# Kernel optimization log

Hardware: AMD Instinct MI355X
Metric: run time of the kernel (lower is better)

Reference implementation:

```python
import jax, jax.numpy as jnp
import numpy as np
import math

B, M, N = 2, 512, 2048
CI = 256          # input_pts_channel == hidden for fuse_method='ADD'
HID = 256
HEADS = 8
DH = HID // HEADS
INTER = 1024
L = 4
EPS = 1e-5


def _ln(x, g, b):
    m = jnp.mean(x, -1, keepdims=True)
    v = jnp.mean((x - m) ** 2, -1, keepdims=True)
    return (x - m) / jnp.sqrt(v + EPS) * g + b


def _sinenc(dims, coords):
    # coords: (B, P) -> (B, P, dims); even channels sin, odd channels cos
    h = jnp.arange(dims)
    inv = jnp.power(10000.0, (h // 2) * 2.0 / dims)
    c = coords[..., None] / inv
    return jnp.where(h % 2 == 0, jnp.sin(c), jnp.cos(c))


def setup_inputs() -> dict:
    key = jax.random.key(0)
    ks = jax.random.split(key, 32)
    it = iter(ks)
    def nrm(shape, s=1.0):
        return jax.random.normal(next(it), shape, dtype=jnp.float32) * s
    inp = {
        'query_c2d': nrm((B, M, 2), 10.0),
        'query_f2d': nrm((B, M, CI)),
        'query_f3d': nrm((B, M, CI)),
        'key_c2d': nrm((B, N, 2), 10.0),
        'key_f2d': nrm((B, N, CI)),
        'key_f3d': nrm((B, N, CI)),
        'attn_mask': jax.random.bernoulli(next(it), 0.9, (B, N)),
        'ln1_g': jnp.ones((CI,)), 'ln1_b': jnp.zeros((CI,)),
        'dc_W': nrm((CI, HID), 0.02), 'dc_b': jnp.zeros((HID,)),
        'dcln_g': jnp.ones((HID,)), 'dcln_b': jnp.zeros((HID,)),
        'cls_f3d': nrm((HID,)),
        'Wq': nrm((L, HID, HID), 0.02), 'bq': jnp.zeros((L, HID)),
        'Wk': nrm((L, HID, HID), 0.02), 'bk': jnp.zeros((L, HID)),
        'Wv': nrm((L, HID, HID), 0.02), 'bv': jnp.zeros((L, HID)),
        'Wd': nrm((L, HID, HID), 0.02), 'bd': jnp.zeros((L, HID)),
        'aln_g': jnp.ones((L, HID)), 'aln_b': jnp.zeros((L, HID)),
        'W1': nrm((L, HID, INTER), 0.02), 'b1': jnp.zeros((L, INTER)),
        'W2': nrm((L, INTER, HID), 0.02), 'b2': jnp.zeros((L, HID)),
        'fln_g': jnp.ones((L, HID)), 'fln_b': jnp.zeros((L, HID)),
    }
    return inp


def _forward(qc2, qf2, qf3, kc2, kf2, kf3, mask,
             ln1_g, ln1_b, dc_W, dc_b, dcln_g, dcln_b, cls_f3d,
             Wq, bq, Wk, bk, Wv, bv, Wd, bd, aln_g, aln_b,
             W1, b1, W2, b2, fln_g, fln_b):
    def sh(x):  # (B,P,HID) -> (B,H,P,DH)
        return x.reshape(x.shape[0], x.shape[1], HEADS, DH).transpose(0, 2, 1, 3)

    def layer(i, q_in, k_in, m, query_self):
        Qh = sh(q_in @ Wq[i] + bq[i])
        Kh = sh(k_in @ Wk[i] + bk[i])
        Vh = sh(k_in @ Wv[i] + bv[i])
        scores = jnp.einsum('bhmd,bhnd->bhmn', Qh, Kh)
        if m is not None:
            scores = scores - (~m).astype(scores.dtype)[:, None, None, :] * 1e10
        if query_self:
            SKh = sh(q_in @ Wk[i] + bk[i])
            SVh = sh(q_in @ Wv[i] + bv[i])
            sself = jnp.sum(Qh * SKh, -1, keepdims=True)  # (B,H,M,1)
            scores = jnp.concatenate([sself, scores], -1)
        probs = jax.nn.softmax(scores / math.sqrt(DH), -1)
        if query_self:
            sp, probs = probs[..., :1], probs[..., 1:]
        o = jnp.einsum('bhmn,bhnd->bhmd', probs, Vh)
        if query_self:
            o = o + sp * SVh
        o = o.transpose(0, 2, 1, 3).reshape(q_in.shape[0], q_in.shape[1], HID)
        a = _ln(o @ Wd[i] + bd[i] + q_in, aln_g[i], aln_b[i])
        f = jax.nn.relu(a @ W1[i] + b1[i]) @ W2[i] + b2[i]
        return _ln(f + a, fln_g[i], fln_b[i])

    qc = jnp.concatenate([_sinenc(CI // 2, qc2[:, :, 0]), _sinenc(CI // 2, qc2[:, :, 1])], -1)
    kc = jnp.concatenate([_sinenc(CI // 2, kc2[:, :, 0]), _sinenc(CI // 2, kc2[:, :, 1])], -1)
    qs = _ln(_ln(qf2 + qf3 + qc, ln1_g, ln1_b) @ dc_W + dc_b, dcln_g, dcln_b)
    ks = _ln(_ln(kf2 + kf3 + kc, ln1_g, ln1_b) @ dc_W + dc_b, dcln_g, dcln_b)
    cls = jnp.broadcast_to(cls_f3d[None, None, :], (qs.shape[0], 1, HID))
    for i in range(L):
        ks = layer(i, ks, ks, mask, False)
        qs = layer(i, qs, ks, mask, True)
        cls = layer(i, cls, jnp.concatenate([cls, ks, qs], 1), None, False)
    return qs, ks, cls


def reference(query_c2d, query_f2d, query_f3d, key_c2d, key_f2d, key_f3d, attn_mask,
              ln1_g, ln1_b, dc_W, dc_b, dcln_g, dcln_b, cls_f3d,
              Wq, bq, Wk, bk, Wv, bv, Wd, bd, aln_g, aln_b,
              W1, b1, W2, b2, fln_g, fln_b):
    return _forward(query_c2d, query_f2d, query_f3d, key_c2d, key_f2d, key_f3d, attn_mask,
                    ln1_g, ln1_b, dc_W, dc_b, dcln_g, dcln_b, cls_f3d,
                    Wq, bq, Wk, bk, Wv, bv, Wd, bd, aln_g, aln_b,
                    W1, b1, W2, b2, fln_g, fln_b)
```

## Files before the change

### kernel.cpp

```cpp
#include <hip/hip_runtime.h>
#include <math.h>

namespace {
constexpr int kB = 2;
constexpr int kM = 512;
constexpr int kN = 2048;
constexpr int kHID = 256;
constexpr int kDH = 32;
constexpr int kL = 4;
constexpr float kEPS = 1e-5f;
constexpr int kKV = 2560;
}

typedef __attribute__((ext_vector_type(8))) short short8;
typedef __attribute__((ext_vector_type(4))) float f32x4;

__device__ inline ushort f2b(float f) {
  unsigned u = __builtin_bit_cast(unsigned, f);
  unsigned r = (u + 0x7fffu + ((u >> 16) & 1u)) >> 16;
  return (ushort)r;
}
__device__ inline float b2f(ushort u) {
  return __builtin_bit_cast(float, (unsigned)u << 16);
}
__device__ inline unsigned cvtpk(float lo, float hi) {
  unsigned r;
  asm("v_cvt_pk_bf16_f32 %0, %1, %2" : "=v"(r) : "v"(lo), "v"(hi));
  return r;
}
__device__ inline void gld16(ushort* lds, const ushort* g) {
  __builtin_amdgcn_global_load_lds(
      (const __attribute__((address_space(1))) void*)g,
      (__attribute__((address_space(3))) void*)lds, 16, 0, 0);
}

__device__ inline float dot8(const float* a, short8 w) {
  float s = 0.f;
  #pragma unroll
  for (int jj = 0; jj < 8; ++jj) s += a[jj] * b2f((ushort)w[jj]);
  return s;
}

__global__ __launch_bounds__(256) void mask_norm_kernel(
    const unsigned char* __restrict__ mraw, float* __restrict__ mf)
{
  int tid = threadIdx.x;
  __shared__ unsigned sh[4];
  if (tid < 4) sh[tid] = 0;
  __syncthreads();
  unsigned l1 = 0, l2 = 0, l3 = 0, l4 = 0;
  for (int j = 0; j < 16; ++j) {
    int p = tid * 16 + j;
    unsigned v = mraw[p];
    int r = p & 3;
    if (r == 1) l1 |= v;
    else if (r == 2) l2 |= v;
    else if (r == 3) l3 |= v;
    else if ((p & 7) == 4) l4 |= v;
  }
  if (l1) atomicOr(&sh[0], l1);
  if (l2) atomicOr(&sh[1], l2);
  if (l3) atomicOr(&sh[2], l3);
  if (l4) atomicOr(&sh[3], l4);
  __syncthreads();
  unsigned a1 = sh[0], a2 = sh[1], a3 = sh[2], a4 = sh[3];
  int mode;
  if ((a1 | a2 | a3) == 0) mode = a4 ? 1 : 2;
  else if (a1 == 0 && (a2 & ~0x80u) == 0 && (a3 & ~0x3Fu) == 0 && ((a2 | a3) != 0))
    mode = 3;
  else mode = 0;

  int i = blockIdx.x * 256 + tid;
  unsigned char v;
  if (mode == 0) v = mraw[i];
  else if (mode == 1) v = mraw[i * 4];
  else if (mode == 2) v = mraw[i * 8];
  else v = mraw[i * 4 + 3];
  mf[i] = v ? 0.f : -2.5505654e9f;
}

__global__ __launch_bounds__(256) void encode2_kernel(
    const float* __restrict__ qc2, const float* __restrict__ qf2,
    const float* __restrict__ qf3, const float* __restrict__ kc2,
    const float* __restrict__ kf2, const float* __restrict__ kf3,
    const float* __restrict__ g, const float* __restrict__ bb,
    ushort* __restrict__ out)
{
  int row = blockIdx.x;
  const float *c2d, *f2, *f3;
  int r;
  if (row < kB * kM) { c2d = qc2; f2 = qf2; f3 = qf3; r = row; }
  else { c2d = kc2; f2 = kf2; f3 = kf3; r = row - kB * kM; }
  int c = threadIdx.x;
  float coord = c2d[(size_t)r * 2 + (c >> 7)];
  int h = c & 127;
  float ex = (float)(h & ~1) * (1.0f / 128.0f);
  float inv = expf(ex * 9.210340371976184f);
  float val = coord / inv;
  float e = (h & 1) ? cosf(val) : sinf(val);
  float x = f2[(size_t)r * 256 + c] + f3[(size_t)r * 256 + c] + e;
  __shared__ float red[256];
  red[c] = x; __syncthreads();
  for (int s = 128; s > 0; s >>= 1) { if (c < s) red[c] += red[c + s]; __syncthreads(); }
  float mean = red[0] * (1.0f / 256.0f);
  __syncthreads();
  float d = x - mean;
  red[c] = d * d; __syncthreads();
  for (int s = 128; s > 0; s >>= 1) { if (c < s) red[c] += red[c + s]; __syncthreads(); }
  float var = red[0] * (1.0f / 256.0f);
  out[(size_t)row * 256 + c] = f2b(d * rsqrtf(var + kEPS) * g[c] + bb[c]);
}

struct WJobs {
  const float* W[7]; ushort* Wt[7];
  int K[7], C[7], off[7];
};
__global__ __launch_bounds__(256) void wconv_all_kernel(WJobs J)
{
  __shared__ float t[32][33];
  int bid = blockIdx.x;
  int j = 0;
  #pragma unroll
  for (int q = 1; q < 7; ++q) if (bid >= J.off[q]) j = q;
  int tl = bid - J.off[j];
  int K = J.K[j], C = J.C[j];
  int tpl = (K >> 5) * (C >> 5);
  int layer = tl / tpl, rem = tl - layer * tpl;
  int kt = rem % (K >> 5), ct = rem / (K >> 5);
  const float* Wl = J.W[j] + (size_t)layer * K * C;
  ushort* Wtl = J.Wt[j] + (size_t)layer * K * C;
  int k0 = kt * 32, c0 = ct * 32;
  int tx = threadIdx.x & 31, ty = threadIdx.x >> 5;
  for (int i = ty; i < 32; i += 8) t[i][tx] = Wl[(size_t)(k0 + i) * C + c0 + tx];
  __syncthreads();
  for (int i = ty; i < 32; i += 8)
    Wtl[(size_t)(c0 + i) * K + k0 + tx] = f2b(t[tx][i]);
}

struct GDesc {
  const ushort* A; const ushort* Bt; const float* bias; const float* res; void* out;
  int R, K, C, flags;
  int in_rpb, out_rpb, out_off, vt_stride;
};
struct GBatch { GDesc d[5]; };

__global__ __launch_bounds__(256) void gemmx_kernel(GBatch bt)
{
  GDesc d = bt.d[blockIdx.z];
  int r0 = blockIdx.x * 64;
  if (r0 >= d.R) return;
  int c0 = blockIdx.y * 64;

  __shared__ ushort As[4096];
  __shared__ ushort Bs[4096];
  int tid = threadIdx.x;
  int lam = tid & 63, wv = tid >> 6;
  int wr = wv >> 1, wc = wv & 1;
  int K = d.K;
  int srow8 = lam >> 3;
  int sxor = (lam & 7) ^ srow8;

  f32x4 acc[2][2] = {};

  for (int k0 = 0; k0 < K; k0 += 64) {
    #pragma unroll
    for (int i = 0; i < 2; ++i) {
      int row = 16 * wv + 8 * i + srow8;
      gld16(As + wv * 1024 + i * 512,
            d.A + (size_t)(r0 + row) * K + k0 + 8 * sxor);
      gld16(Bs + wv * 1024 + i * 512,
            d.Bt + (size_t)(c0 + row) * K + k0 + 8 * sxor);
    }
    __syncthreads();
    #pragma unroll
    for (int ks = 0; ks < 2; ++ks) {
      short8 af[2], bf_[2];
      #pragma unroll
      for (int m = 0; m < 2; ++m) {
        int ra = wr * 32 + m * 16 + (lam & 15);
        int ch = (ks * 4 + (lam >> 4)) ^ (ra & 7);
        af[m] = *(const short8*)(As + ra * 64 + ch * 8);
      }
      #pragma unroll
      for (int n = 0; n < 2; ++n) {
        int rb = wc * 32 + n * 16 + (lam & 15);
        int ch = (ks * 4 + (lam >> 4)) ^ (rb & 7);
        bf_[n] = *(const short8*)(Bs + rb * 64 + ch * 8);
      }
      #pragma unroll
      for (int m = 0; m < 2; ++m)
        #pragma unroll
        for (int n = 0; n < 2; ++n)
          acc[m][n] = __builtin_amdgcn_mfma_f32_16x16x32_bf16(
              af[m], bf_[n], acc[m][n], 0, 0, 0);
    }
    __syncthreads();
  }

  if (!(d.flags & 4)) {
    #pragma unroll
    for (int m = 0; m < 2; ++m) {
      #pragma unroll
      for (int reg = 0; reg < 4; ++reg) {
        int gr = r0 + wr * 32 + m * 16 + (lam >> 4) * 4 + reg;
        int bidx = gr / d.in_rpb, rr = gr - bidx * d.in_rpb;
        size_t orow = (size_t)bidx * d.out_rpb + d.out_off + rr;
        #pragma unroll
        for (int n = 0; n < 2; ++n) {
          int gc = c0 + wc * 32 + n * 16 + (lam & 15);
          float v = acc[m][n][reg] + d.bias[gc];
          if (d.res) v += d.res[(size_t)gr * d.C + gc];
          if (d.flags & 1) v = fmaxf(v, 0.f);
          if (d.flags & 2) ((ushort*)d.out)[orow * d.C + gc] = f2b(v);
          else ((float*)d.out)[orow * d.C + gc] = v;
        }
      }
    }
  } else {
    #pragma unroll
    for (int m = 0; m < 2; ++m)
      #pragma unroll
      for (int n = 0; n < 2; ++n)
        #pragma unroll
        for (int reg = 0; reg < 4; ++reg) {
          int col = wc * 32 + n * 16 + (lam & 15);
          int row = wr * 32 + m * 16 + (lam >> 4) * 4 + reg;
          float v = acc[m][n][reg] + d.bias[c0 + col];
          As[col * 64 + (((row >> 3) ^ (col & 7)) << 3) + (row & 7)] = f2b(v);
        }
    __syncthreads();
    int col2 = tid >> 2, rc = tid & 3;
    #pragma unroll
    for (int u = 0; u < 2; ++u) {
      int rowc = rc * 2 + u;
      short8 val = *(const short8*)(As + col2 * 64 + ((rowc ^ (col2 & 7)) << 3));
      int r = r0 + rowc * 8;
      int bidx = r / d.in_rpb, rr = r - bidx * d.in_rpb;
      *(short8*)((ushort*)d.out +
                 ((size_t)bidx * 256 + c0 + col2) * d.vt_stride + d.out_off + rr) = val;
    }
  }
}

__global__ __launch_bounds__(256) void gemmln_kernel(
    const ushort* __restrict__ A, const ushort* __restrict__ Bt,
    const float* __restrict__ bias, const float* __restrict__ res,
    const float* __restrict__ g, const float* __restrict__ bb,
    float* __restrict__ outf, ushort* __restrict__ outb, int R, int K)
{
  __shared__ ushort As[16 * 64];
  __shared__ ushort Bs[256 * 64];
  __shared__ float redL[16][4];
  int r0 = blockIdx.x * 16;
  int tid = threadIdx.x;
  int lam = tid & 63, wv = tid >> 6;
  int srow8 = lam >> 3;
  int sxor = (lam & 7) ^ srow8;

  f32x4 acc[4] = {};

  for (int k0 = 0; k0 < K; k0 += 64) {
    if (wv < 2)
      gld16(As + wv * 512, A + (size_t)(r0 + wv * 8 + srow8) * K + k0 + 8 * sxor);
    #pragma unroll
    for (int j = 0; j < 8; ++j) {
      int cc = wv * 8 + j;
      gld16(Bs + cc * 512, Bt + (size_t)(cc * 8 + srow8) * K + k0 + 8 * sxor);
    }
    __syncthreads();
    #pragma unroll
    for (int ks = 0; ks < 2; ++ks) {
      int ra = lam & 15;
      int cha = (ks * 4 + (lam >> 4)) ^ (ra & 7);
      short8 af = *(const short8*)(As + ra * 64 + cha * 8);
      #pragma unroll
      for (int cg = 0; cg < 4; ++cg) {
        int rb = wv * 64 + cg * 16 + (lam & 15);
        int chb = (ks * 4 + (lam >> 4)) ^ (rb & 7);
        short8 bf_ = *(const short8*)(Bs + rb * 64 + chb * 8);
        acc[cg] = __builtin_amdgcn_mfma_f32_16x16x32_bf16(af, bf_, acc[cg], 0, 0, 0);
      }
    }
    __syncthreads();
  }

  int col_lo = lam & 15, rsel = lam >> 4;
  float v[4][4];
  #pragma unroll
  for (int cg = 0; cg < 4; ++cg) {
    int col = wv * 64 + cg * 16 + col_lo;
    float bi = bias[col];
    #pragma unroll
    for (int reg = 0; reg < 4; ++reg) {
      int row = r0 + rsel * 4 + reg;
      float x = acc[cg][reg] + bi;
      if (res) x += res[(size_t)row * 256 + col];
      v[cg][reg] = x;
    }
  }
  float mean[4];
  {
    float ps[4];
    #pragma unroll
    for (int reg = 0; reg < 4; ++reg) {
      ps[reg] = v[0][reg] + v[1][reg] + v[2][reg] + v[3][reg];
      #pragma unroll
      for (int o = 1; o < 16; o <<= 1) ps[reg] += __shfl_xor(ps[reg], o);
    }
    if (col_lo == 0)
      #pragma unroll
      for (int reg = 0; reg < 4; ++reg) redL[rsel * 4 + reg][wv] = ps[reg];
    __syncthreads();
    #pragma unroll
    for (int reg = 0; reg < 4; ++reg) {
      int rr = rsel * 4 + reg;
      mean[reg] = (redL[rr][0] + redL[rr][1] + redL[rr][2] + redL[rr][3]) * (1.0f / 256.0f);
    }
    __syncthreads();
  }
  float rs_[4];
  {
    float ps[4];
    #pragma unroll
    for (int reg = 0; reg < 4; ++reg) {
      float s = 0.f;
      #pragma unroll
      for (int cg = 0; cg < 4; ++cg) {
        float dd = v[cg][reg] - mean[reg];
        s += dd * dd;
      }
      ps[reg] = s;
      #pragma unroll
      for (int o = 1; o < 16; o <<= 1) ps[reg] += __shfl_xor(ps[reg], o);
    }
    if (col_lo == 0)
      #pragma unroll
      for (int reg = 0; reg < 4; ++reg) redL[rsel * 4 + reg][wv] = ps[reg];
    __syncthreads();
    #pragma unroll
    for (int reg = 0; reg < 4; ++reg) {
      int rr = rsel * 4 + reg;
      float var = (redL[rr][0] + redL[rr][1] + redL[rr][2] + redL[rr][3]) * (1.0f / 256.0f);
      rs_[reg] = rsqrtf(var + kEPS);
    }
  }
  #pragma unroll
  for (int cg = 0; cg < 4; ++cg) {
    int col = wv * 64 + cg * 16 + col_lo;
    float gg = g[col], bv = bb[col];
    #pragma unroll
    for (int reg = 0; reg < 4; ++reg) {
      int row = r0 + rsel * 4 + reg;
      float y = (v[cg][reg] - mean[reg]) * rs_[reg] * gg + bv;
      outf[(size_t)row * 256 + col] = y;
      outb[(size_t)row * 256 + col] = f2b(y);
    }
  }
}

__global__ __launch_bounds__(256) void attn6_kernel(
    const ushort* __restrict__ Qp, const ushort* __restrict__ Kp,
    const ushort* __restrict__ Vt, float* __restrict__ Pp,
    const float* __restrict__ madd,
    int Sq, int k_rpb, int vt_stride, int self_off, int slen, int ns)
{
  __shared__ ushort KsL[64 * 32];
  __shared__ ushort VtL[32 * 64];
  int bh = blockIdx.x;
  int b = bh >> 3, h = bh & 7;
  int sidx = blockIdx.z;
  int tid = threadIdx.x;
  int lane = tid & 63;
  int qlane = lane & 15, g = lane >> 4;
  int gq = blockIdx.y * 64 + (tid >> 6) * 16 + qlane;
  const float scale2 = 0.17677669529663688f * 1.4426950408889634f;

  short8 qB = *(const short8*)(Qp + ((size_t)(b * Sq + gq)) * 256 + h * 32 + g * 8);

  float mi = -3.0e38f, li = 0.f;
  f32x4 acc0 = {}, acc1 = {};

  if (self_off >= 0 && sidx == 0) {
    const ushort* kr = Kp + ((size_t)(b * k_rpb + self_off + gq)) * 256 + h * 32 + g * 8;
    short8 k8 = *(const short8*)kr;
    float part = 0.f;
    #pragma unroll
    for (int j = 0; j < 8; ++j) part += b2f((ushort)qB[j]) * b2f((ushort)k8[j]);
    part += __shfl_xor(part, 16);
    part += __shfl_xor(part, 32);
    mi = part * scale2;
    li = 1.f;
    const ushort* vb = Vt + ((size_t)(b * 256 + h * 32)) * vt_stride + self_off + gq;
    #pragma unroll
    for (int r = 0; r < 4; ++r) {
      acc0[r] = b2f(vb[(size_t)(4 * g + r) * vt_stride]);
      acc1[r] = b2f(vb[(size_t)(16 + 4 * g + r) * vt_stride]);
    }
  }

  const float* mb = madd + (size_t)b * kN;
  int skey = tid >> 2, sc = tid & 3;
  int sd = tid >> 3, sc8 = tid & 7;
  const ushort* Ksrc = Kp + ((size_t)(b * k_rpb + skey)) * 256 + h * 32 + sc * 8;
  const ushort* Vsrc = Vt + ((size_t)(b * 256 + h * 32 + sd)) * vt_stride + sc8 * 8;
  ushort* Kdst = KsL + skey * 32 + ((sc ^ ((skey >> 1) & 3)) << 3);
  ushort* Vdst = VtL + sd * 64 + ((sc8 ^ (sd & 7)) << 3);

  int base = sidx * slen;
  int ntile = slen >> 6;

  for (int it = 0; it < ntile; ++it) {
    int n0 = base + it * 64;
    __syncthreads();
    *(short8*)Kdst = *(const short8*)(Ksrc + (size_t)n0 * 256);
    *(short8*)Vdst = *(const short8*)(Vsrc + n0);
    __syncthreads();

    float4 m4[4];
    #pragma unroll
    for (int f = 0; f < 4; ++f)
      m4[f] = *(const float4*)(mb + n0 + 16 * f + 4 * g);

    f32x4 st[4];
    __builtin_amdgcn_s_setprio(1);
    #pragma unroll
    for (int f = 0; f < 4; ++f) {
      int key = f * 16 + qlane;
      short8 kf = *(const short8*)(KsL + key * 32 + ((g ^ ((key >> 1) & 3)) << 3));
      st[f] = __builtin_amdgcn_mfma_f32_16x16x32_bf16(
          kf, qB, (f32x4){0.f, 0.f, 0.f, 0.f}, 0, 0, 0);
    }
    __builtin_amdgcn_s_setprio(0);

    float p[4][4];
    float tm = -3.0e38f;
    #pragma unroll
    for (int f = 0; f < 4; ++f) {
      float mm[4] = {m4[f].x, m4[f].y, m4[f].z, m4[f].w};
      #pragma unroll
      for (int r = 0; r < 4; ++r) {
        float s = fmaf(st[f][r], scale2, mm[r]);
        p[f][r] = s;
        tm = fmaxf(tm, s);
      }
    }
    tm = fmaxf(tm, __shfl_xor(tm, 16));
    tm = fmaxf(tm, __shfl_xor(tm, 32));
    if (__any(tm > mi + 11.5f)) {
      float nm = fmaxf(mi, tm);
      float fs = exp2f(mi - nm);
      li *= fs; mi = nm;
      #pragma unroll
      for (int r = 0; r < 4; ++r) { acc0[r] *= fs; acc1[r] *= fs; }
    }
    float ls = 0.f;
    #pragma unroll
    for (int f = 0; f < 4; ++f)
      #pragma unroll
      for (int r = 0; r < 4; ++r) {
        float pv = exp2f(p[f][r] - mi);
        p[f][r] = pv;
        ls += pv;
      }
    ls += __shfl_xor(ls, 16);
    ls += __shfl_xor(ls, 32);
    li += ls;

    unsigned pkw[4][2];
    #pragma unroll
    for (int f = 0; f < 4; ++f) {
      pkw[f][0] = cvtpk(p[f][0], p[f][1]);
      pkw[f][1] = cvtpk(p[f][2], p[f][3]);
    }
    int src0 = qlane | ((2 * (g & 1)) << 4);
    int src1 = src0 + 16;
    bool hi = g >= 2;
    #pragma unroll
    for (int t = 0; t < 2; ++t) {
      unsigned t0 = (unsigned)__shfl((int)pkw[2 * t][0], src0);
      unsigned t1 = (unsigned)__shfl((int)pkw[2 * t][1], src0);
      unsigned t2 = (unsigned)__shfl((int)pkw[2 * t][0], src1);
      unsigned t3 = (unsigned)__shfl((int)pkw[2 * t][1], src1);
      unsigned u0 = (unsigned)__shfl((int)pkw[2 * t + 1][0], src0);
      unsigned u1 = (unsigned)__shfl((int)pkw[2 * t + 1][1], src0);
      unsigned u2 = (unsigned)__shfl((int)pkw[2 * t + 1][0], src1);
      unsigned u3 = (unsigned)__shfl((int)pkw[2 * t + 1][1], src1);
      union { unsigned u[4]; short8 v; } pb;
      pb.u[0] = hi ? u0 : t0;
      pb.u[1] = hi ? u1 : t1;
      pb.u[2] = hi ? u2 : t2;
      pb.u[3] = hi ? u3 : t3;
      __builtin_amdgcn_s_setprio(1);
      int d0 = qlane, d1 = 16 + qlane;
      short8 vf0 = *(const short8*)(VtL + d0 * 64 + (((t * 4 + g) ^ (d0 & 7)) << 3));
      acc0 = __builtin_amdgcn_mfma_f32_16x16x32_bf16(vf0, pb.v, acc0, 0, 0, 0);
      short8 vf1 = *(const short8*)(VtL + d1 * 64 + (((t * 4 + g) ^ (d1 & 7)) << 3));
      acc1 = __builtin_amdgcn_mfma_f32_16x16x32_bf16(vf1, pb.v, acc1, 0, 0, 0);
      __builtin_amdgcn_s_setprio(0);
    }
  }

  float* rec = Pp + ((size_t)(bh * Sq + gq) * ns + sidx) * 20;
  if (g == 0) { rec[0] = mi; rec[1] = li; }
  ushort* accp = (ushort*)(rec + 2);
  uint2 w0, w1;
  w0.x = cvtpk(acc0[0], acc0[1]); w0.y = cvtpk(acc0[2], acc0[3]);
  w1.x = cvtpk(acc1[0], acc1[1]); w1.y = cvtpk(acc1[2], acc1[3]);
  *(uint2*)(accp + 4 * g) = w0;
  *(uint2*)(accp + 16 + 4 * g) = w1;
}

__global__ __launch_bounds__(256) void combine_kernel(
    const float* __restrict__ Pp, ushort* __restrict__ AO, int Sq, int ns)
{
  int r = blockIdx.x * 8 + (threadIdx.x >> 5);
  int d = threadIdx.x & 31;
  int bh = r / Sq, q = r - bh * Sq;
  int b = bh >> 3, h = bh & 7;
  const float* rb = Pp + (size_t)r * ns * 20;
  float M = -3.0e38f;
  for (int s2 = 0; s2 < ns; ++s2) M = fmaxf(M, rb[s2 * 20]);
  float L = 0.f, O = 0.f;
  for (int s2 = 0; s2 < ns; ++s2) {
    float w = exp2f(rb[s2 * 20] - M);
    L += rb[s2 * 20 + 1] * w;
    O += w * b2f(((const ushort*)(rb + s2 * 20 + 2))[d]);
  }
  AO[((size_t)(b * Sq + q)) * 256 + h * 32 + d] = f2b(O / L);
}

__global__ __launch_bounds__(256) void cls_attn_kernel(
    const float* __restrict__ cls_s,
    const ushort* __restrict__ WqT, const float* __restrict__ bq,
    const ushort* __restrict__ WkT, const float* __restrict__ bk,
    const ushort* __restrict__ WvT, const float* __restrict__ bv,
    const ushort* __restrict__ Kbig, const ushort* __restrict__ Vt,
    float* __restrict__ AOc)
{
  __shared__ float c0f[256], qv[32], k0v[32], v0v[32];
  __shared__ float red[256];
  __shared__ float sarr[2560];
  __shared__ float scl[4];
  const float scale2 = 0.17677669529663688f * 1.4426950408889634f;
  int b = blockIdx.x >> 3, h = blockIdx.x & 7;
  int t = threadIdx.x;
  c0f[t] = cls_s[b * 256 + t];
  __syncthreads();

  const ushort* Wm[3] = {WqT, WkT, WvT};
  const float* Bi[3] = {bq, bk, bv};
  float* Ov[3] = {qv, k0v, v0v};
  for (int pi = 0; pi < 3; ++pi) {
    int d = t >> 3, sl = t & 7;
    const ushort* wrow = Wm[pi] + (size_t)(h * 32 + d) * 256 + sl * 32;
    float part = 0.f;
    #pragma unroll
    for (int j = 0; j < 32; j += 8) {
      short8 w8 = *(const short8*)(wrow + j);
      #pragma unroll
      for (int jj = 0; jj < 8; ++jj) part += c0f[sl * 32 + j + jj] * b2f((ushort)w8[jj]);
    }
    red[t] = part;
    __syncthreads();
    if (t < 32) {
      float sum = 0.f;
      #pragma unroll
      for (int s = 0; s < 8; ++s) sum += red[t * 8 + s];
      Ov[pi][t] = sum + Bi[pi][h * 32 + t];
    }
    __syncthreads();
  }

  if (t < 32) red[t] = qv[t] * k0v[t];
  __syncthreads();
  if (t == 0) {
    float sc = 0.f;
    for (int j = 0; j < 32; ++j) sc += red[j];
    scl[0] = sc * scale2;
  }
  __syncthreads();

  float lmax = -3.0e38f;
  for (int it = 0; it < 10; ++it) {
    int key = t + it * 256;
    const ushort* krow = Kbig + ((size_t)(b * kKV + key)) * 256 + h * 32;
    float sdot = 0.f;
    #pragma unroll
    for (int j = 0; j < 4; ++j) {
      short8 k8 = ((const short8*)krow)[j];
      #pragma unroll
      for (int jj = 0; jj < 8; ++jj) sdot += qv[j * 8 + jj] * b2f((ushort)k8[jj]);
    }
    sdot *= scale2;
    sarr[key] = sdot;
    lmax = fmaxf(lmax, sdot);
  }
  red[t] = lmax;
  __syncthreads();
  for (int s = 128; s > 0; s >>= 1) { if (t < s) red[t] = fmaxf(red[t], red[t + s]); __syncthreads(); }
  if (t == 0) scl[1] = fmaxf(red[0], scl[0]);
  __syncthreads();
  float M = scl[1];
  float lsum = 0.f;
  for (int it = 0; it < 10; ++it) {
    int key = t + it * 256;
    float pv = exp2f(sarr[key] - M);
    sarr[key] = pv;
    lsum += pv;
  }
  red[t] = lsum;
  __syncthreads();
  for (int s = 128; s > 0; s >>= 1) { if (t < s) red[t] += red[t + s]; __syncthreads(); }
  if (t == 0) {
    scl[3] = exp2f(scl[0] - M);
    scl[2] = red[0] + scl[3];
  }
  __syncthreads();

  {
    int d = t & 31, sl = t >> 5;
    const ushort* vrow = Vt + ((size_t)(b * 256 + h * 32 + d)) * kKV + sl * 320;
    float acc = 0.f;
    for (int j = 0; j < 320; j += 8) {
      short8 v8 = *(const short8*)(vrow + j);
      #pragma unroll
      for (int jj = 0; jj < 8; ++jj) acc += sarr[sl * 320 + j + jj] * b2f((ushort)v8[jj]);
    }
    red[sl * 32 + d] = acc;
  }
  __syncthreads();
  if (t < 32) {
    float o = scl[3] * v0v[t];
    #pragma unroll
    for (int s = 0; s < 8; ++s) o += red[s * 32 + t];
    AOc[b * 256 + h * 32 + t] = o / scl[2];
  }
}

__device__ inline float blk_sum1024(float v, float* red, int t) {
  red[t] = v; __syncthreads();
  for (int s = 512; s > 0; s >>= 1) {
    if (t < s) red[t] += red[t + s];
    __syncthreads();
  }
  float r = red[0];
  __syncthreads();
  return r;
}

__global__ __launch_bounds__(1024) void cls_mlp_kernel(
    const float* __restrict__ AOc, float* __restrict__ cls_s,
    const ushort* __restrict__ WdT, const float* __restrict__ bd,
    const float* __restrict__ ag, const float* __restrict__ ab,
    const ushort* __restrict__ W1T, const float* __restrict__ b1,
    const ushort* __restrict__ W2T, const float* __restrict__ b2,
    const float* __restrict__ fg, const float* __restrict__ fb)
{
  __shared__ float oL[256], r0L[256], aL[256], ffL[1024], vL[256], red[1024];
  int b = blockIdx.x, t = threadIdx.x;
  if (t < 256) { oL[t] = AOc[b * 256 + t]; r0L[t] = cls_s[b * 256 + t]; }
  __syncthreads();

  int r8 = t >> 3, c8 = t & 7;
  #pragma unroll
  for (int p = 0; p < 2; ++p) {
    int row = p * 128 + r8;
    const ushort* wr_ = WdT + (size_t)row * 256 + c8 * 8;
    float a0 = 0.f, a1 = 0.f, a2 = 0.f, a3 = 0.f;
    a0 = dot8(oL + c8 * 8, *(const short8*)(wr_));
    a1 = dot8(oL + c8 * 8 + 64, *(const short8*)(wr_ + 64));
    a2 = dot8(oL + c8 * 8 + 128, *(const short8*)(wr_ + 128));
    a3 = dot8(oL + c8 * 8 + 192, *(const short8*)(wr_ + 192));
    float s = (a0 + a1) + (a2 + a3);
    s += __shfl_xor(s, 1);
    s += __shfl_xor(s, 2);
    s += __shfl_xor(s, 4);
    if (c8 == 0) vL[row] = s + bd[row] + r0L[row];
  }
  __syncthreads();
  {
    float x = (t < 256) ? vL[t] : 0.f;
    float mean = blk_sum1024(x, red, t) * (1.0f / 256.0f);
    float d = (t < 256) ? (vL[t] - mean) : 0.f;
    float var = blk_sum1024(d * d, red, t) * (1.0f / 256.0f);
    float rs = rsqrtf(var + kEPS);
    if (t < 256) aL[t] = d * rs * ag[t] + ab[t];
  }
  __syncthreads();
  #pragma unroll
  for (int p = 0; p < 8; ++p) {
    int row = p * 128 + r8;
    const ushort* w1r = W1T + (size_t)row * 256 + c8 * 8;
    float a0 = dot8(aL + c8 * 8, *(const short8*)(w1r));
    float a1 = dot8(aL + c8 * 8 + 64, *(const short8*)(w1r + 64));
    float a2 = dot8(aL + c8 * 8 + 128, *(const short8*)(w1r + 128));
    float a3 = dot8(aL + c8 * 8 + 192, *(const short8*)(w1r + 192));
    float s = (a0 + a1) + (a2 + a3);
    s += __shfl_xor(s, 1);
    s += __shfl_xor(s, 2);
    s += __shfl_xor(s, 4);
    if (c8 == 0) ffL[row] = fmaxf(s + b1[row], 0.f);
  }
  __syncthreads();
  #pragma unroll
  for (int p = 0; p < 2; ++p) {
    int row = p * 128 + r8;
    const ushort* w2r = W2T + (size_t)row * 1024 + c8 * 8;
    float a0 = 0.f, a1 = 0.f, a2 = 0.f, a3 = 0.f;
    #pragma unroll
    for (int j = 0; j < 1024; j += 256) {
      a0 += dot8(ffL + c8 * 8 + j, *(const short8*)(w2r + j));
      a1 += dot8(ffL + c8 * 8 + j + 64, *(const short8*)(w2r + j + 64));
      a2 += dot8(ffL + c8 * 8 + j + 128, *(const short8*)(w2r + j + 128));
      a3 += dot8(ffL + c8 * 8 + j + 192, *(const short8*)(w2r + j + 192));
    }
    float s = (a0 + a1) + (a2 + a3);
    s += __shfl_xor(s, 1);
    s += __shfl_xor(s, 2);
    s += __shfl_xor(s, 4);
    if (c8 == 0) vL[row] = s + b2[row] + aL[row];
  }
  __syncthreads();
  {
    float x = (t < 256) ? vL[t] : 0.f;
    float mean = blk_sum1024(x, red, t) * (1.0f / 256.0f);
    float d = (t < 256) ? (vL[t] - mean) : 0.f;
    float var = blk_sum1024(d * d, red, t) * (1.0f / 256.0f);
    float rs = rsqrtf(var + kEPS);
    if (t < 256) cls_s[b * 256 + t] = d * rs * fg[t] + fb[t];
  }
}

__global__ void cls_init_kernel(const float* __restrict__ cf, float* __restrict__ cls)
{
  int i = blockIdx.x * 256 + threadIdx.x;
  cls[i] = cf[i & 255];
}

__global__ __launch_bounds__(256) void copyout_kernel(
    const float* __restrict__ qs, const float* __restrict__ ks,
    const float* __restrict__ cls, float* __restrict__ out)
{
  int i = blockIdx.x * 256 + threadIdx.x;
  float v;
  if (i < 262144) v = qs[i];
  else if (i < 1310720) v = ks[i - 262144];
  else v = cls[i - 1310720];
  out[i] = v;
}

extern "C" void kernel_launch(void* const* d_in, const int* in_sizes, int n_in,
                              void* d_out, int out_size, void* d_ws, size_t ws_size,
                              hipStream_t stream)
{
  const float* qc2    = (const float*)d_in[0];
  const float* qf2    = (const float*)d_in[1];
  const float* qf3    = (const float*)d_in[2];
  const float* kc2    = (const float*)d_in[3];
  const float* kf2    = (const float*)d_in[4];
  const float* kf3    = (const float*)d_in[5];
  const unsigned char* mraw = (const unsigned char*)d_in[6];
  const float* ln1_g  = (const float*)d_in[7];
  const float* ln1_b  = (const float*)d_in[8];
  const float* dc_W   = (const float*)d_in[9];
  const float* dc_b   = (const float*)d_in[10];
  const float* dcln_g = (const float*)d_in[11];
  const float* dcln_b = (const float*)d_in[12];
  const float* cls_f  = (const float*)d_in[13];
  const float* Wq     = (const float*)d_in[14];
  const float* bq     = (const float*)d_in[15];
  const float* Wk     = (const float*)d_in[16];
  const float* bk     = (const float*)d_in[17];
  const float* Wv     = (const float*)d_in[18];
  const float* bv     = (const float*)d_in[19];
  const float* Wd     = (const float*)d_in[20];
  const float* bd     = (const float*)d_in[21];
  const float* aln_g  = (const float*)d_in[22];
  const float* aln_b  = (const float*)d_in[23];
  const float* W1     = (const float*)d_in[24];
  const float* b1     = (const float*)d_in[25];
  const float* W2     = (const float*)d_in[26];
  const float* b2     = (const float*)d_in[27];
  const float* fln_g  = (const float*)d_in[28];
  const float* fln_b  = (const float*)d_in[29];

  float* ws = (float*)d_ws;
  float* maskf = ws + 0;
  float* qs_s  = ws + 4096;
  float* ks_s  = ws + 266240;
  float* cls_s = ws + 1314816;
  float* AOc   = ws + 1315328;
  float* Scr   = ws + 1316864;
  float* Ta    = Scr;
  float* ksPart = Scr + 1048576;
  float* qsPart = Scr + 1048576;
  ushort* ub   = (ushort*)(ws + 4986880);
  ushort* qs_b   = ub + 0;
  ushort* ks_b   = ub + 262144;
  ushort* T2b    = ub + 1310720;
  ushort* Kbig   = ub + 2359296;
  ushort* Vt_ks  = ub + 3670016;
  ushort* Vt_big = ub + 4718592;
  ushort* FFb    = ub + 6029312;
  ushort* encT   = FFb + 0;
  ushort* Qb     = FFb + 0;
  ushort* Kks    = FFb + 1048576;
  ushort* AOb    = FFb + 2097152;
  ushort* wts    = ub + 10223616;
  ushort* dcWt = wts;
  ushort* WqT  = wts + 65536;
  ushort* WkT  = WqT + 262144;
  ushort* WvT  = WkT + 262144;
  ushort* WdT  = WvT + 262144;
  ushort* W1T  = WdT + 262144;
  ushort* W2T  = W1T + 1048576;

  auto mk = [](const ushort* A, const ushort* Bt, const float* bias, const float* res,
               void* out, int R, int K, int C, int flags,
               int in_rpb, int out_rpb, int out_off, int vt_stride) {
    GDesc g; g.A = A; g.Bt = Bt; g.bias = bias; g.res = res; g.out = out;
    g.R = R; g.K = K; g.C = C; g.flags = flags; g.in_rpb = in_rpb;
    g.out_rpb = out_rpb; g.out_off = out_off; g.vt_stride = vt_stride; return g;
  };
  auto launch = [&](const GDesc* ds, int n) {
    GBatch bt{};
    int maxR = 0;
    for (int i = 0; i < n; ++i) { bt.d[i] = ds[i]; if (ds[i].R > maxR) maxR = ds[i].R; }
    gemmx_kernel<<<dim3(maxR / 64, ds[0].C / 64, n), 256, 0, stream>>>(bt);
  };
  auto gln = [&](const ushort* A, const ushort* Bt, const float* bias, const float* res,
                 const float* g_, const float* b_, float* of, ushort* ob, int R, int K) {
    gemmln_kernel<<<R / 16, 256, 0, stream>>>(A, Bt, bias, res, g_, b_, of, ob, R, K);
  };

  mask_norm_kernel<<<16, 256, 0, stream>>>(mraw, maskf);

  {
    WJobs J;
    const float* Ws[7] = {dc_W, Wq, Wk, Wv, Wd, W1, W2};
    ushort* Ts[7] = {dcWt, WqT, WkT, WvT, WdT, W1T, W2T};
    int Ks[7] = {256, 256, 256, 256, 256, 256, 1024};
    int Cs[7] = {256, 256, 256, 256, 256, 1024, 256};
    int Ls[7] = {1, 4, 4, 4, 4, 4, 4};
    int off = 0;
    for (int j = 0; j < 7; ++j) {
      J.W[j] = Ws[j]; J.Wt[j] = Ts[j]; J.K[j] = Ks[j]; J.C[j] = Cs[j]; J.off[j] = off;
      off += (Ks[j] / 32) * (Cs[j] / 32) * Ls[j];
    }
    wconv_all_kernel<<<off, 256, 0, stream>>>(J);
  }

  encode2_kernel<<<kB * (kM + kN), 256, 0, stream>>>(qc2, qf2, qf3, kc2, kf2, kf3,
                                                     ln1_g, ln1_b, encT);
  gln(encT, dcWt, dc_b, nullptr, dcln_g, dcln_b, qs_s, qs_b, kB * (kM + kN), 256);
  cls_init_kernel<<<2, 256, 0, stream>>>(cls_f, cls_s);

  for (int i = 0; i < kL; ++i) {
    const ushort* Wq_i = WqT + (size_t)i * 65536;  const float* bq_i = bq + i * 256;
    const ushort* Wk_i = WkT + (size_t)i * 65536;  const float* bk_i = bk + i * 256;
    const ushort* Wv_i = WvT + (size_t)i * 65536;  const float* bv_i = bv + i * 256;
    const ushort* Wd_i = WdT + (size_t)i * 65536;  const float* bd_i = bd + i * 256;
    const float* ag_i = aln_g + i * 256;           const float* ab_i = aln_b + i * 256;
    const ushort* W1_i = W1T + (size_t)i * 262144; const float* b1_i = b1 + i * 1024;
    const ushort* W2_i = W2T + (size_t)i * 262144; const float* b2_i = b2 + i * 256;
    const float* fg_i = fln_g + i * 256;           const float* fb_i = fln_b + i * 256;
    int Rk = kB * kN, Rq = kB * kM;

    {
      GDesc ds[3] = {
        mk(ks_b, Wq_i, bq_i, nullptr, Qb,  Rk, 256, 256, 2, Rk, Rk, 0, 0),
        mk(ks_b, Wk_i, bk_i, nullptr, Kks, Rk, 256, 256, 2, Rk, Rk, 0, 0),
        mk(ks_b, Wv_i, bv_i, nullptr, Vt_ks, Rk, 256, 256, 4, kN, 0, 0, kN)};
      launch(ds, 3);
    }
    attn6_kernel<<<dim3(kB * 8, kN / 64, 4), 256, 0, stream>>>(
        Qb, Kks, Vt_ks, ksPart, maskf, kN, kN, kN, -1, kN / 4, 4);
    combine_kernel<<<kB * 8 * kN / 8, 256, 0, stream>>>(ksPart, AOb, kN, 4);
    gln(AOb, Wd_i, bd_i, ks_s, ag_i, ab_i, Ta, T2b, Rk, 256);
    { GDesc d = mk(T2b, W1_i, b1_i, nullptr, FFb, Rk, 256, 1024, 1 | 2, Rk, Rk, 0, 0);
      launch(&d, 1); }
    gln(FFb, W2_i, b2_i, Ta, fg_i, fb_i, ks_s, ks_b, Rk, 1024);

    {
      GDesc ds[5] = {
        mk(qs_b, Wq_i, bq_i, nullptr, Qb, Rq, 256, 256, 2, Rq, Rq, 0, 0),
        mk(ks_b, Wk_i, bk_i, nullptr, Kbig, Rk, 256, 256, 2, kN, kKV, 0, 0),
        mk(ks_b, Wv_i, bv_i, nullptr, Vt_big, Rk, 256, 256, 4, kN, 0, 0, kKV),
        mk(qs_b, Wk_i, bk_i, nullptr, Kbig, Rq, 256, 256, 2, kM, kKV, kN, 0),
        mk(qs_b, Wv_i, bv_i, nullptr, Vt_big, Rq, 256, 256, 4, kM, 0, kN, kKV)};
      launch(ds, 5);
    }
    attn6_kernel<<<dim3(kB * 8, kM / 64, 4), 256, 0, stream>>>(
        Qb, Kbig, Vt_big, qsPart, maskf, kM, kKV, kKV, kN, kN / 4, 4);
    combine_kernel<<<kB * 8 * kM / 8, 256, 0, stream>>>(qsPart, AOb, kM, 4);
    gln(AOb, Wd_i, bd_i, qs_s, ag_i, ab_i, Ta, T2b, Rq, 256);
    { GDesc d = mk(T2b, W1_i, b1_i, nullptr, FFb, Rq, 256, 1024, 1 | 2, Rq, Rq, 0, 0);
      launch(&d, 1); }
    gln(FFb, W2_i, b2_i, Ta, fg_i, fb_i, qs_s, qs_b, Rq, 1024);

    {
      GDesc ds[2] = {
        mk(qs_b, Wk_i, bk_i, nullptr, Kbig, Rq, 256, 256, 2, kM, kKV, kN, 0),
        mk(qs_b, Wv_i, bv_i, nullptr, Vt_big, Rq, 256, 256, 4, kM, 0, kN, kKV)};
      launch(ds, 2);
    }
    cls_attn_kernel<<<16, 256, 0, stream>>>(cls_s, Wq_i, bq_i, Wk_i,
                                            bk_i, Wv_i, bv_i,
                                            Kbig, Vt_big, AOc);
    cls_mlp_kernel<<<2, 1024, 0, stream>>>(AOc, cls_s, Wd_i, bd_i, ag_i, ab_i,
                                           W1_i, b1_i, W2_i, b2_i, fg_i, fb_i);
  }

  copyout_kernel<<<5122, 256, 0, stream>>>(qs_s, ks_s, cls_s, (float*)d_out);
}
```

Baseline: 831.6 us.

## Process two query groups per wave to reuse K/V tiles in attention

The attention kernel now gives each wave two 16-query groups, so a block covers 128 queries and each K/V tile staged in LDS feeds twice as many MFMAs. This halves the number of blocks and the global-to-LDS traffic per query. The query-side attention also raises its KV split count from 4 to 8 to keep the grid large, with the combine step adjusted to match. The cost is roughly double the accumulator and score registers, which may lower occupancy, plus more partial records to merge for the query attention.

After: 837.7 us. No clear change (+0.7%).

```diff
diff --git a/kernel.cpp b/kernel.cpp
--- a/kernel.cpp
+++ b/kernel.cpp
@@ -358,7 +358,7 @@
   }
 }
 
-__global__ __launch_bounds__(256) void attn6_kernel(
+__global__ __launch_bounds__(256) void attn8_kernel(
     const ushort* __restrict__ Qp, const ushort* __restrict__ Kp,
     const ushort* __restrict__ Vt, float* __restrict__ Pp,
     const float* __restrict__ madd,
@@ -372,29 +372,48 @@
   int tid = threadIdx.x;
   int lane = tid & 63;
   int qlane = lane & 15, g = lane >> 4;
-  int gq = blockIdx.y * 64 + (tid >> 6) * 16 + qlane;
+  int gqA = blockIdx.y * 128 + (tid >> 6) * 16 + qlane;
+  int gqB = gqA + 64;
   const float scale2 = 0.17677669529663688f * 1.4426950408889634f;
 
-  short8 qB = *(const short8*)(Qp + ((size_t)(b * Sq + gq)) * 256 + h * 32 + g * 8);
-
-  float mi = -3.0e38f, li = 0.f;
-  f32x4 acc0 = {}, acc1 = {};
+  short8 qBa = *(const short8*)(Qp + ((size_t)(b * Sq + gqA)) * 256 + h * 32 + g * 8);
+  short8 qBb = *(const short8*)(Qp + ((size_t)(b * Sq + gqB)) * 256 + h * 32 + g * 8);
+
+  float miA = -3.0e38f, liA = 0.f, miB = -3.0e38f, liB = 0.f;
+  f32x4 a0A = {}, a1A = {}, a0B = {}, a1B = {};
 
   if (self_off >= 0 && sidx == 0) {
-    const ushort* kr = Kp + ((size_t)(b * k_rpb + self_off + gq)) * 256 + h * 32 + g * 8;
-    short8 k8 = *(const short8*)kr;
-    float part = 0.f;
-    #pragma unroll
-    for (int j = 0; j < 8; ++j) part += b2f((ushort)qB[j]) * b2f((ushort)k8[j]);
-    part += __shfl_xor(part, 16);
-    part += __shfl_xor(part, 32);
-    mi = part * scale2;
-    li = 1.f;
-    const ushort* vb = Vt + ((size_t)(b * 256 + h * 32)) * vt_stride + self_off + gq;
-    #pragma unroll
-    for (int r = 0; r < 4; ++r) {
-      acc0[r] = b2f(vb[(size_t)(4 * g + r) * vt_stride]);
-      acc1[r] = b2f(vb[(size_t)(16 + 4 * g + r) * vt_stride]);
+    {
+      const ushort* kr = Kp + ((size_t)(b * k_rpb + self_off + gqA)) * 256 + h * 32 + g * 8;
+      short8 k8 = *(const short8*)kr;
+      float part = 0.f;
+      #pragma unroll
+      for (int j = 0; j < 8; ++j) part += b2f((ushort)qBa[j]) * b2f((ushort)k8[j]);
+      part += __shfl_xor(part, 16);
+      part += __shfl_xor(part, 32);
+      miA = part * scale2; liA = 1.f;
+      const ushort* vb = Vt + ((size_t)(b * 256 + h * 32)) * vt_stride + self_off + gqA;
+      #pragma unroll
+      for (int r = 0; r < 4; ++r) {
+        a0A[r] = b2f(vb[(size_t)(4 * g + r) * vt_stride]);
+        a1A[r] = b2f(vb[(size_t)(16 + 4 * g + r) * vt_stride]);
+      }
+    }
+    {
+      const ushort* kr = Kp + ((size_t)(b * k_rpb + self_off + gqB)) * 256 + h * 32 + g * 8;
+      short8 k8 = *(const short8*)kr;
+      float part = 0.f;
+      #pragma unroll
+      for (int j = 0; j < 8; ++j) part += b2f((ushort)qBb[j]) * b2f((ushort)k8[j]);
+      part += __shfl_xor(part, 16);
+      part += __shfl_xor(part, 32);
+      miB = part * scale2; liB = 1.f;
+      const ushort* vb = Vt + ((size_t)(b * 256 + h * 32)) * vt_stride + self_off + gqB;
+      #pragma unroll
+      for (int r = 0; r < 4; ++r) {
+        a0B[r] = b2f(vb[(size_t)(4 * g + r) * vt_stride]);
+        a1B[r] = b2f(vb[(size_t)(16 + 4 * g + r) * vt_stride]);
+      }
     }
   }
 
@@ -409,6 +428,10 @@
   int base = sidx * slen;
   int ntile = slen >> 6;
 
+  int src0 = qlane | ((2 * (g & 1)) << 4);
+  int src1 = src0 + 16;
+  bool hi = g >= 2;
+
   for (int it = 0; it < ntile; ++it) {
     int n0 = base + it * 64;
     __syncthreads();
@@ -421,93 +444,164 @@
     for (int f = 0; f < 4; ++f)
       m4[f] = *(const float4*)(mb + n0 + 16 * f + 4 * g);
 
-    f32x4 st[4];
+    f32x4 stA[4], stB[4];
     __builtin_amdgcn_s_setprio(1);
     #pragma unroll
     for (int f = 0; f < 4; ++f) {
       int key = f * 16 + qlane;
       short8 kf = *(const short8*)(KsL + key * 32 + ((g ^ ((key >> 1) & 3)) << 3));
-      st[f] = __builtin_amdgcn_mfma_f32_16x16x32_bf16(
-          kf, qB, (f32x4){0.f, 0.f, 0.f, 0.f}, 0, 0, 0);
+      stA[f] = __builtin_amdgcn_mfma_f32_16x16x32_bf16(
+          kf, qBa, (f32x4){0.f, 0.f, 0.f, 0.f}, 0, 0, 0);
+      stB[f] = __builtin_amdgcn_mfma_f32_16x16x32_bf16(
+          kf, qBb, (f32x4){0.f, 0.f, 0.f, 0.f}, 0, 0, 0);
     }
     __builtin_amdgcn_s_setprio(0);
 
-    float p[4][4];
-    float tm = -3.0e38f;
-    #pragma unroll
-    for (int f = 0; f < 4; ++f) {
-      float mm[4] = {m4[f].x, m4[f].y, m4[f].z, m4[f].w};
-      #pragma unroll
-      for (int r = 0; r < 4; ++r) {
-        float s = fmaf(st[f][r], scale2, mm[r]);
-        p[f][r] = s;
-        tm = fmaxf(tm, s);
-      }
-    }
-    tm = fmaxf(tm, __shfl_xor(tm, 16));
-    tm = fmaxf(tm, __shfl_xor(tm, 32));
-    if (__any(tm > mi + 11.5f)) {
-      float nm = fmaxf(mi, tm);
-      float fs = exp2f(mi - nm);
-      li *= fs; mi = nm;
-      #pragma unroll
-      for (int r = 0; r < 4; ++r) { acc0[r] *= fs; acc1[r] *= fs; }
-    }
-    float ls = 0.f;
-    #pragma unroll
-    for (int f = 0; f < 4; ++f)
-      #pragma unroll
-      for (int r = 0; r < 4; ++r) {
-        float pv = exp2f(p[f][r] - mi);
-        p[f][r] = pv;
-        ls += pv;
-      }
-    ls += __shfl_xor(ls, 16);
-    ls += __shfl_xor(ls, 32);
-    li += ls;
-
-    unsigned pkw[4][2];
-    #pragma unroll
-    for (int f = 0; f < 4; ++f) {
-      pkw[f][0] = cvtpk(p[f][0], p[f][1]);
-      pkw[f][1] = cvtpk(p[f][2], p[f][3]);
-    }
-    int src0 = qlane | ((2 * (g & 1)) << 4);
-    int src1 = src0 + 16;
-    bool hi = g >= 2;
+    unsigned pkwA[4][2], pkwB[4][2];
+    {
+      float p[4][4];
+      float tm = -3.0e38f;
+      #pragma unroll
+      for (int f = 0; f < 4; ++f) {
+        float mm[4] = {m4[f].x, m4[f].y, m4[f].z, m4[f].w};
+        #pragma unroll
+        for (int r = 0; r < 4; ++r) {
+          float sv = fmaf(stA[f][r], scale2, mm[r]);
+          p[f][r] = sv;
+          tm = fmaxf(tm, sv);
+        }
+      }
+      tm = fmaxf(tm, __shfl_xor(tm, 16));
+      tm = fmaxf(tm, __shfl_xor(tm, 32));
+      if (__any(tm > miA + 11.5f)) {
+        float nm = fmaxf(miA, tm);
+        float fs = exp2f(miA - nm);
+        liA *= fs; miA = nm;
+        #pragma unroll
+        for (int r = 0; r < 4; ++r) { a0A[r] *= fs; a1A[r] *= fs; }
+      }
+      float ls = 0.f;
+      #pragma unroll
+      for (int f = 0; f < 4; ++f)
+        #pragma unroll
+        for (int r = 0; r < 4; ++r) {
+          float pv = exp2f(p[f][r] - miA);
+          p[f][r] = pv;
+          ls += pv;
+        }
+      ls += __shfl_xor(ls, 16);
+      ls += __shfl_xor(ls, 32);
+      liA += ls;
+      #pragma unroll
+      for (int f = 0; f < 4; ++f) {
+        pkwA[f][0] = cvtpk(p[f][0], p[f][1]);
+        pkwA[f][1] = cvtpk(p[f][2], p[f][3]);
+      }
+    }
+    {
+      float p[4][4];
+      float tm = -3.0e38f;
+      #pragma unroll
+      for (int f = 0; f < 4; ++f) {
+        float mm[4] = {m4[f].x, m4[f].y, m4[f].z, m4[f].w};
+        #pragma unroll
+        for (int r = 0; r < 4; ++r) {
+          float sv = fmaf(stB[f][r], scale2, mm[r]);
+          p[f][r] = sv;
+          tm = fmaxf(tm, sv);
+        }
+      }
+      tm = fmaxf(tm, __shfl_xor(tm, 16));
+      tm = fmaxf(tm, __shfl_xor(tm, 32));
+      if (__any(tm > miB + 11.5f)) {
+        float nm = fmaxf(miB, tm);
+        float fs = exp2f(miB - nm);
+        liB *= fs; miB = nm;
+        #pragma unroll
+        for (int r = 0; r < 4; ++r) { a0B[r] *= fs; a1B[r] *= fs; }
+      }
+      float ls = 0.f;
+      #pragma unroll
+      for (int f = 0; f < 4; ++f)
+        #pragma unroll
+        for (int r = 0; r < 4; ++r) {
+          float pv = exp2f(p[f][r] - miB);
+          p[f][r] = pv;
+          ls += pv;
+        }
+      ls += __shfl_xor(ls, 16);
+      ls += __shfl_xor(ls, 32);
+      liB += ls;
+      #pragma unroll
+      for (int f = 0; f < 4; ++f) {
+        pkwB[f][0] = cvtpk(p[f][0], p[f][1]);
+        pkwB[f][1] = cvtpk(p[f][2], p[f][3]);
+      }
+    }
+
     #pragma unroll
     for (int t = 0; t < 2; ++t) {
-      unsigned t0 = (unsigned)__shfl((int)pkw[2 * t][0], src0);
-      unsigned t1 = (unsigned)__shfl((int)pkw[2 * t][1], src0);
-      unsigned t2 = (unsigned)__shfl((int)pkw[2 * t][0], src1);
-      unsigned t3 = (unsigned)__shfl((int)pkw[2 * t][1], src1);
-      unsigned u0 = (unsigned)__shfl((int)pkw[2 * t + 1][0], src0);
-      unsigned u1 = (unsigned)__shfl((int)pkw[2 * t + 1][1], src0);
-      unsigned u2 = (unsigned)__shfl((int)pkw[2 * t + 1][0], src1);
-      unsigned u3 = (unsigned)__shfl((int)pkw[2 * t + 1][1], src1);
-      union { unsigned u[4]; short8 v; } pb;
-      pb.u[0] = hi ? u0 : t0;
-      pb.u[1] = hi ? u1 : t1;
-      pb.u[2] = hi ? u2 : t2;
-      pb.u[3] = hi ? u3 : t3;
+      union { unsigned u[4]; short8 v; } pbA, pbB;
+      {
+        unsigned t0 = (unsigned)__shfl((int)pkwA[2 * t][0], src0);
+        unsigned t1 = (unsigned)__shfl((int)pkwA[2 * t][1], src0);
+        unsigned t2 = (unsigned)__shfl((int)pkwA[2 * t][0], src1);
+        unsigned t3 = (unsigned)__shfl((int)pkwA[2 * t][1], src1);
+        unsigned u0 = (unsigned)__shfl((int)pkwA[2 * t + 1][0], src0);
+        unsigned u1 = (unsigned)__shfl((int)pkwA[2 * t + 1][1], src0);
+        unsigned u2 = (unsigned)__shfl((int)pkwA[2 * t + 1][0], src1);
+        unsigned u3 = (unsigned)__shfl((int)pkwA[2 * t + 1][1], src1);
+        pbA.u[0] = hi ? u0 : t0;
+        pbA.u[1] = hi ? u1 : t1;
+        pbA.u[2] = hi ? u2 : t2;
+        pbA.u[3] = hi ? u3 : t3;
+      }
+      {
+        unsigned t0 = (unsigned)__shfl((int)pkwB[2 * t][0], src0);
+        unsigned t1 = (unsigned)__shfl((int)pkwB[2 * t][1], src0);
+        unsigned t2 = (unsigned)__shfl((int)pkwB[2 * t][0], src1);
+        unsigned t3 = (unsigned)__shfl((int)pkwB[2 * t][1], src1);
+        unsigned u0 = (unsigned)__shfl((int)pkwB[2 * t + 1][0], src0);
+        unsigned u1 = (unsigned)__shfl((int)pkwB[2 * t + 1][1], src0);
+        unsigned u2 = (unsigned)__shfl((int)pkwB[2 * t + 1][0], src1);
+        unsigned u3 = (unsigned)__shfl((int)pkwB[2 * t + 1][1], src1);
+        pbB.u[0] = hi ? u0 : t0;
+        pbB.u[1] = hi ? u1 : t1;
+        pbB.u[2] = hi ? u2 : t2;
+        pbB.u[3] = hi ? u3 : t3;
+      }
       __builtin_amdgcn_s_setprio(1);
       int d0 = qlane, d1 = 16 + qlane;
       short8 vf0 = *(const short8*)(VtL + d0 * 64 + (((t * 4 + g) ^ (d0 & 7)) << 3));
-      acc0 = __builtin_amdgcn_mfma_f32_16x16x32_bf16(vf0, pb.v, acc0, 0, 0, 0);
       short8 vf1 = *(const short8*)(VtL + d1 * 64 + (((t * 4 + g) ^ (d1 & 7)) << 3));
-      acc1 = __builtin_amdgcn_mfma_f32_16x16x32_bf16(vf1, pb.v, acc1, 0, 0, 0);
+      a0A = __builtin_amdgcn_mfma_f32_16x16x32_bf16(vf0, pbA.v, a0A, 0, 0, 0);
+      a1A = __builtin_amdgcn_mfma_f32_16x16x32_bf16(vf1, pbA.v, a1A, 0, 0, 0);
+      a0B = __builtin_amdgcn_mfma_f32_16x16x32_bf16(vf0, pbB.v, a0B, 0, 0, 0);
+      a1B = __builtin_amdgcn_mfma_f32_16x16x32_bf16(vf1, pbB.v, a1B, 0, 0, 0);
       __builtin_amdgcn_s_setprio(0);
     }
   }
 
-  float* rec = Pp + ((size_t)(bh * Sq + gq) * ns + sidx) * 20;
-  if (g == 0) { rec[0] = mi; rec[1] = li; }
-  ushort* accp = (ushort*)(rec + 2);
-  uint2 w0, w1;
-  w0.x = cvtpk(acc0[0], acc0[1]); w0.y = cvtpk(acc0[2], acc0[3]);
-  w1.x = cvtpk(acc1[0], acc1[1]); w1.y = cvtpk(acc1[2], acc1[3]);
-  *(uint2*)(accp + 4 * g) = w0;
-  *(uint2*)(accp + 16 + 4 * g) = w1;
+  {
+    float* rec = Pp + ((size_t)(bh * Sq + gqA) * ns + sidx) * 20;
+    if (g == 0) { rec[0] = miA; rec[1] = liA; }
+    ushort* accp = (ushort*)(rec + 2);
+    uint2 w0, w1;
+    w0.x = cvtpk(a0A[0], a0A[1]); w0.y = cvtpk(a0A[2], a0A[3]);
+    w1.x = cvtpk(a1A[0], a1A[1]); w1.y = cvtpk(a1A[2], a1A[3]);
+    *(uint2*)(accp + 4 * g) = w0;
+    *(uint2*)(accp + 16 + 4 * g) = w1;
+  }
+  {
+    float* rec = Pp + ((size_t)(bh * Sq + gqB) * ns + sidx) * 20;
+    if (g == 0) { rec[0] = miB; rec[1] = liB; }
+    ushort* accp = (ushort*)(rec + 2);
+    uint2 w0, w1;
+    w0.x = cvtpk(a0B[0], a0B[1]); w0.y = cvtpk(a0B[2], a0B[3]);
+    w1.x = cvtpk(a1B[0], a1B[1]); w1.y = cvtpk(a1B[2], a1B[3]);
+    *(uint2*)(accp + 4 * g) = w0;
+    *(uint2*)(accp + 16 + 4 * g) = w1;
+  }
 }
 
 __global__ __launch_bounds__(256) void combine_kernel(
@@ -873,7 +967,7 @@
         mk(ks_b, Wv_i, bv_i, nullptr, Vt_ks, Rk, 256, 256, 4, kN, 0, 0, kN)};
       launch(ds, 3);
     }
-    attn6_kernel<<<dim3(kB * 8, kN / 64, 4), 256, 0, stream>>>(
+    attn8_kernel<<<dim3(kB * 8, kN / 128, 4), 256, 0, stream>>>(
         Qb, Kks, Vt_ks, ksPart, maskf, kN, kN, kN, -1, kN / 4, 4);
     combine_kernel<<<kB * 8 * kN / 8, 256, 0, stream>>>(ksPart, AOb, kN, 4);
     gln(AOb, Wd_i, bd_i, ks_s, ag_i, ab_i, Ta, T2b, Rk, 256);
@@ -890,9 +984,9 @@
         mk(qs_b, Wv_i, bv_i, nullptr, Vt_big, Rq, 256, 256, 4, kM, 0, kN, kKV)};
       launch(ds, 5);
     }
-    attn6_kernel<<<dim3(kB * 8, kM / 64, 4), 256, 0, stream>>>(
-        Qb, Kbig, Vt_big, qsPart, maskf, kM, kKV, kKV, kN, kN / 4, 4);
-    combine_kernel<<<kB * 8 * kM / 8, 256, 0, stream>>>(qsPart, AOb, kM, 4);
+    attn8_kernel<<<dim3(kB * 8, kM / 128, 8), 256, 0, stream>>>(
+        Qb, Kbig, Vt_big, qsPart, maskf, kM, kKV, kKV, kN, kN / 8, 8);
+    combine_kernel<<<kB * 8 * kM / 8, 256, 0, stream>>>(qsPart, AOb, kM, 8);
     gln(AOb, Wd_i, bd_i, qs_s, ag_i, ab_i, Ta, T2b, Rq, 256);
     { GDesc d = mk(T2b, W1_i, b1_i, nullptr, FFb, Rq, 256, 1024, 1 | 2, Rq, Rq, 0, 0);
       launch(&d, 1); }
```
